# Kernel tuning notes

Hardware: AMD Instinct MI355X
Metric: run time of the kernel (lower is better)

## Reference

```python
import jax, jax.numpy as jnp
import numpy as np

EPS = 1e-5  # pyg LayerNorm default eps


def _graph_ln(x):
    # pyg.nn.norm.LayerNorm(affine=False), default mode='graph', batch=None:
    # normalizes over ALL elements of the tensor (x - x.mean()) / x.std(unbiased=False)
    m = x.mean()
    v = jnp.mean((x - m) ** 2)
    return (x - m) * jax.lax.rsqrt(v + EPS)


def _cheb_conv(x, row, col, w, W, b):
    # ChebConv, normalization='sym', lambda_max=2 => scaled Laplacian
    # L_hat = L - I = -D^{-1/2} A D^{-1/2} (self-loops removed, weighted)
    # x: [B,N,C_in], row/col: [E], w: [E], W: [K,C_in,C_out], b: [C_out]
    N = x.shape[1]
    w = jnp.where(row == col, 0.0, w)  # remove_self_loops
    deg = jnp.zeros((N,), x.dtype).at[row].add(w)
    dinv = jnp.where(deg > 0, jax.lax.rsqrt(jnp.maximum(deg, 1e-12)), 0.0)
    norm = -(dinv[row] * w * dinv[col])  # [E]

    def prop(t):  # out[i] += norm_e * t[j] for edge (j=row -> i=col)
        msg = norm[None, :, None] * t[:, row, :]  # [B,E,C]
        return jnp.zeros_like(t).at[:, col, :].add(msg)

    Tx0 = x
    out = jnp.einsum('bnc,cd->bnd', Tx0, W[0])
    Tx1 = prop(x)
    out = out + jnp.einsum('bnc,cd->bnd', Tx1, W[1])
    for k in range(2, W.shape[0]):
        Tx2 = 2.0 * prop(Tx1) - Tx0
        out = out + jnp.einsum('bnc,cd->bnd', Tx2, W[k])
        Tx0, Tx1 = Tx1, Tx2
    return out + b


def setup_inputs() -> dict:
    key = jax.random.key(0)
    ks = jax.random.split(key, 8)
    B, N, C, E, L, K = 8, 2048, 256, 32768, 3, 3
    node_feature = jax.random.normal(ks[0], (B, N, C), dtype=jnp.float32)
    edge_index = jax.random.randint(ks[1], (L, 2, E), 0, N)
    edge_weight = jax.random.uniform(ks[2], (L, E), dtype=jnp.float32)
    s = 1.0 / np.sqrt(C)
    cheb_w = jax.random.normal(ks[3], (L, K, C, C), dtype=jnp.float32) * s
    cheb_b = jnp.zeros((L, C), dtype=jnp.float32)
    mlp_w = jax.random.normal(ks[4], (L, C, C), dtype=jnp.float32) * s
    mlp_b = jax.random.normal(ks[5], (L, C), dtype=jnp.float32) * 0.01
    return {"node_feature": node_feature, "edge_weight": edge_weight,
            "cheb_w": cheb_w, "cheb_b": cheb_b, "mlp_w": mlp_w,
            "mlp_b": mlp_b, "edge_index": edge_index}


def reference(node_feature, edge_weight, cheb_w, cheb_b, mlp_w, mlp_b, edge_index):
    h = node_feature  # [B,N,C]
    L = cheb_w.shape[0]
    for l in range(L):
        h_res = h
        hn = _graph_ln(h)
        hc = _cheb_conv(hn, edge_index[l, 0], edge_index[l, 1],
                        edge_weight[l], cheb_w[l], cheb_b[l])
        h = hc + h_res
        h_res = h
        hn = _graph_ln(h)
        hm = jax.nn.gelu(jnp.einsum('bnc,cd->bnd', hn, mlp_w[l]) + mlp_b[l],
                         approximate=False)  # dropout is identity at inference
        h = hm + h_res
    return h.mean(axis=1)  # [B,C]
```

## Files before the change

### kernel.cpp

```cpp
#include <hip/hip_runtime.h>

#define BATCH   8
#define NNODE   2048
#define CH      256
#define NEDGE   32768
#define NLAYER  3
#define MROWS   (NNODE*BATCH)
#define KCAT    (3*CH)
#define NTOT    (MROWS*CH)

typedef _Float16 half8 __attribute__((ext_vector_type(8)));
typedef _Float16 half4 __attribute__((ext_vector_type(4)));
typedef float    f32x4 __attribute__((ext_vector_type(4)));

#define OFF_ACAT   ((size_t)0)
#define OFF_HF     ((size_t)25165824)
#define OFF_WT     ((size_t)33554432)
#define OFF_MT     ((size_t)34734080)
#define OFF_PARTA  ((size_t)35127296)
#define OFF_PARTB  ((size_t)35135488)
#define OFF_CS     ((size_t)35143680)
#define OFF_CSM    ((size_t)35152896)
#define OFF_DEG    ((size_t)35155968)
#define OFF_CNT    ((size_t)35180544)
#define OFF_ELIST  ((size_t)35205120)
#define OFF_NORM   ((size_t)36777984)
#define OFF_R1     ((size_t)37171200)
#define OFF_R2     ((size_t)37195776)
#define OFF_MP     ((size_t)37220352)

__device__ __forceinline__ void async_lds16(const void* g, void* l) {
  __builtin_amdgcn_global_load_lds((const __attribute__((address_space(1))) void*)g,
                                   (__attribute__((address_space(3))) void*)l, 16, 0, 0);
}

__global__ __launch_bounds__(256) void k_init(const float* __restrict__ x,
                                              _Float16* __restrict__ Acat,
                                              float2* __restrict__ part,
                                              const float* __restrict__ cheb_w,
                                              const float* __restrict__ mlp_w,
                                              _Float16* __restrict__ Wt,
                                              _Float16* __restrict__ Mt,
                                              float* __restrict__ deg,
                                              unsigned int* __restrict__ count,
                                              float* __restrict__ r1) {
  __shared__ float rs[512];
  __shared__ _Float16 lt[64][72];
  const int blk = blockIdx.x, t = threadIdx.x;
  if (blk < 1024) {
    int tid = blk*256 + t;
    float s = 0.f, s2 = 0.f;
    for (int i = tid; i < NTOT/4; i += 1024*256) {
      int c4 = i & 63, b = (i >> 6) & 7, n = i >> 9;
      float4 v = ((const float4*)x)[((b*NNODE + n) << 6) + c4];
      half4 o; o[0]=(_Float16)v.x; o[1]=(_Float16)v.y; o[2]=(_Float16)v.z; o[3]=(_Float16)v.w;
      *(half4*)&Acat[(size_t)(i >> 6)*KCAT + c4*4] = o;
      s  += v.x + v.y + v.z + v.w;
      s2 += v.x*v.x + v.y*v.y + v.z*v.z + v.w*v.w;
    }
    rs[t] = s; rs[256+t] = s2; __syncthreads();
    for (int o = 128; o > 0; o >>= 1) {
      if (t < o) { rs[t] += rs[t+o]; rs[256+t] += rs[256+t+o]; }
      __syncthreads();
    }
    if (t == 0) part[blk] = make_float2(rs[0], rs[256]);
  } else if (blk < 1048) {
    int i = (blk - 1024)*256 + t;
    if (i < NLAYER*NNODE) { deg[i] = 0.f; count[i] = 0u; r1[i] = 0.f; }
  } else {
    const int tile = blk - 1048;
    const int rr = t >> 4, c4 = t & 15;
    if (tile < 144) {
      const int l = tile / 48, rem = tile % 48;
      const int kk = rem / 16, q = rem % 16, ci = q >> 2, ni = q & 3;
      const float4* W  = (const float4*)cheb_w + ((size_t)((l*3 + kk)*CH + ci*64))*64 + ni*16;
      const float4* W2 = (const float4*)cheb_w + ((size_t)((l*3 + 2 )*CH + ci*64))*64 + ni*16;
      #pragma unroll
      for (int p = 0; p < 4; ++p) {
        const int r = p*16 + rr;
        float4 v = W[(size_t)r*64 + c4];
        if (kk == 0) {
          float4 v2 = W2[(size_t)r*64 + c4];
          v.x -= v2.x; v.y -= v2.y; v.z -= v2.z; v.w -= v2.w;
        } else if (kk == 2) {
          v.x *= 2.f; v.y *= 2.f; v.z *= 2.f; v.w *= 2.f;
        }
        lt[c4*4+0][r] = (_Float16)v.x; lt[c4*4+1][r] = (_Float16)v.y;
        lt[c4*4+2][r] = (_Float16)v.z; lt[c4*4+3][r] = (_Float16)v.w;
      }
      __syncthreads();
      const int nr = t >> 2, ch2 = t & 3;
      #pragma unroll
      for (int pp = 0; pp < 2; ++pp) {
        const int ch = ch2 + pp*4;
        half8 v = *(const half8*)&lt[nr][ch*8];
        *(half8*)&Wt[((size_t)(l*CH + ni*64 + nr))*KCAT + kk*256 + ci*64 + ch*8] = v;
      }
    } else {
      const int m = tile - 144;
      const int l = m / 16, q = m % 16, ci = q >> 2, ni = q & 3;
      const float4* W = (const float4*)mlp_w + ((size_t)(l*CH + ci*64))*64 + ni*16;
      #pragma unroll
      for (int p = 0; p < 4; ++p) {
        const int r = p*16 + rr;
        float4 v = W[(size_t)r*64 + c4];
        lt[c4*4+0][r] = (_Float16)v.x; lt[c4*4+1][r] = (_Float16)v.y;
        lt[c4*4+2][r] = (_Float16)v.z; lt[c4*4+3][r] = (_Float16)v.w;
      }
      __syncthreads();
      const int nr = t >> 2, ch2 = t & 3;
      #pragma unroll
      for (int pp = 0; pp < 2; ++pp) {
        const int ch = ch2 + pp*4;
        half8 v = *(const half8*)&lt[nr][ch*8];
        *(half8*)&Mt[((size_t)(l*CH + ni*64 + nr))*CH + ci*64 + ch*8] = v;
      }
    }
  }
}

__global__ __launch_bounds__(256) void k_edge_scatter(const int* __restrict__ ei,
                                                      const float* __restrict__ ew,
                                                      float* deg, unsigned int* count,
                                                      unsigned int* elist) {
  int i = blockIdx.x*256 + threadIdx.x;
  if (i >= NLAYER*NEDGE) return;
  int l = i / NEDGE, e = i % NEDGE;
  const int* rows = ei + l*2*NEDGE;
  const int* cols = rows + NEDGE;
  int r = rows[e], c = cols[e];
  float w = (r == c) ? 0.f : ew[i];
  atomicAdd(&deg[l*NNODE + r], w);
  unsigned int slot = atomicAdd(&count[l*NNODE + c], 1u);
  if (slot < 64u) elist[(size_t)(l*NNODE + c)*64 + slot] = (unsigned int)e;
}

__global__ __launch_bounds__(256) void k_edge_norm(const int* __restrict__ ei,
                                                   const float* __restrict__ ew,
                                                   const float* __restrict__ deg,
                                                   float* __restrict__ norm,
                                                   float* __restrict__ r1) {
  int i = blockIdx.x*256 + threadIdx.x;
  if (i >= NLAYER*NEDGE) return;
  int l = i / NEDGE, e = i % NEDGE;
  const int* rows = ei + l*2*NEDGE;
  const int* cols = rows + NEDGE;
  int r = rows[e], c = cols[e];
  float w = (r == c) ? 0.f : ew[i];
  float dr = deg[l*NNODE + r], dc = deg[l*NNODE + c];
  float ir = dr > 0.f ? rsqrtf(fmaxf(dr, 1e-12f)) : 0.f;
  float ic = dc > 0.f ? rsqrtf(fmaxf(dc, 1e-12f)) : 0.f;
  float nm = -(ir * w * ic);
  norm[i] = nm;
  atomicAdd(&r1[l*NNODE + c], nm);
}

__global__ __launch_bounds__(256) void k_aux(const int* __restrict__ ei,
                                             const float* __restrict__ norm,
                                             const unsigned int* __restrict__ count,
                                             const unsigned int* __restrict__ elist,
                                             const float* __restrict__ r1,
                                             float* __restrict__ r2,
                                             const _Float16* __restrict__ Wt,
                                             const _Float16* __restrict__ Mt,
                                             float* __restrict__ cs,
                                             float* __restrict__ csM) {
  const int blk = blockIdx.x;
  if (blk < 24) {
    int i = blk*256 + threadIdx.x;
    int l = i / NNODE;
    const int* rows = ei + l*2*NEDGE;
    unsigned int c = count[i]; if (c > 64u) c = 64u;
    const unsigned int* el = elist + (size_t)i*64;
    float s = 0.f;
    for (unsigned int j = 0; j < c; ++j) {
      unsigned int e = el[j];
      s += norm[l*NEDGE + e] * r1[l*NNODE + rows[e]];
    }
    r2[i] = s;
  } else if (blk < 33) {
    int idx = blk - 24;
    int l = idx / 3, kk = idx % 3, n = threadIdx.x;
    const half8* row = (const half8*)&Wt[((size_t)(l*CH + n))*KCAT + kk*256];
    float s = 0.f;
    #pragma unroll 4
    for (int j = 0; j < 32; ++j) {
      half8 v = row[j];
      s += (float)v[0]+(float)v[1]+(float)v[2]+(float)v[3]
         + (float)v[4]+(float)v[5]+(float)v[6]+(float)v[7];
    }
    cs[(l*3 + kk)*CH + n] = s;
  } else {
    int l = blk - 33, n = threadIdx.x;
    const half8* row = (const half8*)&Mt[((size_t)(l*CH + n))*CH];
    float s = 0.f;
    #pragma unroll 4
    for (int j = 0; j < 32; ++j) {
      half8 v = row[j];
      s += (float)v[0]+(float)v[1]+(float)v[2]+(float)v[3]
         + (float)v[4]+(float)v[5]+(float)v[6]+(float)v[7];
    }
    csM[l*CH + n] = s;
  }
}

template<int SRC_OFF, int DST_OFF>
__global__ __launch_bounds__(256) void k_prop(_Float16* __restrict__ Acat,
                                              const int* __restrict__ rows,
                                              const float* __restrict__ nrm,
                                              const unsigned int* __restrict__ count,
                                              const unsigned int* __restrict__ el) {
  const int g = blockIdx.x*4 + (threadIdx.x >> 6);
  const int lane = threadIdx.x & 63;
  const int dst = g >> 1, bb = (g & 1) << 2;
  unsigned int c = count[dst]; if (c > 64u) c = 64u;
  int srcv = 0; float nmv = 0.f;
  if (lane < (int)c) {
    unsigned int e = el[(size_t)dst*64 + lane];
    srcv = rows[e]; nmv = nrm[e];
  }
  float acc[4][4] = {{0.f,0.f,0.f,0.f},{0.f,0.f,0.f,0.f},{0.f,0.f,0.f,0.f},{0.f,0.f,0.f,0.f}};
  const _Float16* base = Acat + SRC_OFF + lane*4;
  for (unsigned int i = 0; i < c; ++i) {
    int   src = __builtin_amdgcn_readlane(srcv, i);
    int   nbi = __builtin_amdgcn_readlane(__builtin_bit_cast(int, nmv), i);
    float nm  = __builtin_bit_cast(float, nbi);
    const _Float16* p = base + (size_t)(src*8 + bb)*KCAT;
    #pragma unroll
    for (int j = 0; j < 4; ++j) {
      half4 v = *(const half4*)(p + (size_t)j*KCAT);
      acc[j][0] += nm*(float)v[0]; acc[j][1] += nm*(float)v[1];
      acc[j][2] += nm*(float)v[2]; acc[j][3] += nm*(float)v[3];
    }
  }
  #pragma unroll
  for (int j = 0; j < 4; ++j) {
    half4 o; o[0]=(_Float16)acc[j][0]; o[1]=(_Float16)acc[j][1];
    o[2]=(_Float16)acc[j][2]; o[3]=(_Float16)acc[j][3];
    *(half4*)&Acat[(size_t)(dst*8 + bb + j)*KCAT + DST_OFF + lane*4] = o;
  }
}

template<int KSTEPS, int DO_GELU>
__global__ __launch_bounds__(256) void k_gemm(const _Float16* __restrict__ A, int lda,
                                              const _Float16* __restrict__ Bt, int ldb,
                                              const float* __restrict__ bias,
                                              const float* __restrict__ cs,
                                              const float* __restrict__ r1,
                                              const float* __restrict__ r2,
                                              const float2* __restrict__ part_in,
                                              float2* __restrict__ part_out,
                                              const _Float16* __restrict__ R, int ldr,
                                              _Float16* __restrict__ O, int ldo) {
  __shared__ _Float16 Als[64*64];
  __shared__ _Float16 Bls[64*64];
  __shared__ float red[512];
  __shared__ float mv[2];
  const int bm = blockIdx.x, bn = blockIdx.y;
  const int t = threadIdx.x;
  const int w = t >> 6, lane = t & 63;
  const int quad = lane >> 4, l16 = lane & 15;
  const int wm = w & 1, wn = w >> 1;

  {
    float s = 0.f, s2 = 0.f;
    for (int i = t; i < 1024; i += 256) { float2 p = part_in[i]; s += p.x; s2 += p.y; }
    red[t] = s; red[256+t] = s2; __syncthreads();
    for (int o = 128; o > 0; o >>= 1) {
      if (t < o) { red[t] += red[t+o]; red[256+t] += red[256+t+o]; }
      __syncthreads();
    }
    if (t == 0) {
      float mean = red[0] * (1.f/(float)NTOT);
      float var  = red[256] * (1.f/(float)NTOT) - mean*mean;
      mv[0] = mean; mv[1] = rsqrtf(var + 1e-5f);
    }
    __syncthreads();
  }
  const float mean = mv[0], istd = mv[1];

  f32x4 acc00 = {0.f,0.f,0.f,0.f};
  f32x4 acc01 = acc00, acc10 = acc00, acc11 = acc00;

  const int c0 = w*64 + lane, c1 = 256 + w*64 + lane;
  const int r0 = c0 >> 3, s0 = (c0 & 7) ^ (r0 & 7);
  const int r1i = c1 >> 3, s1 = (c1 & 7) ^ (r1i & 7);
  const _Float16* ga0 = A  + (size_t)(bm*64 + r0)*lda + s0*8;
  const _Float16* ga1 = A  + (size_t)(bm*64 + r1i)*lda + s1*8;
  const _Float16* gb0 = Bt + (size_t)(bn*64 + r0)*ldb + s0*8;
  const _Float16* gb1 = Bt + (size_t)(bn*64 + r1i)*ldb + s1*8;
  _Float16* lA0 = &Als[w*512];
  _Float16* lA1 = &Als[2048 + w*512];
  _Float16* lB0 = &Bls[w*512];
  _Float16* lB1 = &Bls[2048 + w*512];

  const int ra0 = wm*32 + l16, ra1 = ra0 + 16;
  const int rb0 = wn*32 + l16, rb1 = rb0 + 16;

  for (int ks = 0; ks < KSTEPS; ++ks) {
    async_lds16(ga0, lA0); async_lds16(ga1, lA1);
    async_lds16(gb0, lB0); async_lds16(gb1, lB1);
    ga0 += 64; ga1 += 64; gb0 += 64; gb1 += 64;
    __syncthreads();
    #pragma unroll
    for (int kh = 0; kh < 2; ++kh) {
      const int q = kh*4 + quad;
      half8 a0 = *(const half8*)&Als[ra0*64 + (q ^ (ra0 & 7))*8];
      half8 a1 = *(const half8*)&Als[ra1*64 + (q ^ (ra1 & 7))*8];
      half8 b0 = *(const half8*)&Bls[rb0*64 + (q ^ (rb0 & 7))*8];
      half8 b1 = *(const half8*)&Bls[rb1*64 + (q ^ (rb1 & 7))*8];
      acc00 = __builtin_amdgcn_mfma_f32_16x16x32_f16(a0, b0, acc00, 0, 0, 0);
      acc01 = __builtin_amdgcn_mfma_f32_16x16x32_f16(a0, b1, acc01, 0, 0, 0);
      acc10 = __builtin_amdgcn_mfma_f32_16x16x32_f16(a1, b0, acc10, 0, 0, 0);
      acc11 = __builtin_amdgcn_mfma_f32_16x16x32_f16(a1, b1, acc11, 0, 0, 0);
    }
    __syncthreads();
  }

  float s = 0.f, s2 = 0.f;
  const int gm0 = bm*64 + wm*32, gn0 = bn*64 + wn*32;
  const float mi = -mean * istd;
  #pragma unroll
  for (int i = 0; i < 2; ++i) {
    #pragma unroll
    for (int j = 0; j < 2; ++j) {
      f32x4 a = (i == 0) ? (j == 0 ? acc00 : acc01) : (j == 0 ? acc10 : acc11);
      const int col = gn0 + j*16 + l16;
      const float bv = bias[col];
      const float c0v = cs[col];
      float c1v = 0.f, c2v = 0.f;
      if (!DO_GELU) { c1v = cs[256 + col]; c2v = cs[512 + col]; }
      #pragma unroll
      for (int r = 0; r < 4; ++r) {
        const int row = gm0 + i*16 + quad*4 + r;
        float v;
        if (DO_GELU) {
          v = istd*a[r] + mi*c0v + bv;
          v = 0.5f*v*(1.f + erff(v*0.70710678118654752f));
        } else {
          const int node = row >> 3;
          v = istd*a[r] + mi*(c0v + r1[node]*c1v + r2[node]*c2v) + bv;
        }
        float hv = (float)R[(size_t)row*ldr + col] + v;
        O[(size_t)row*ldo + col] = (_Float16)hv;
        s += hv; s2 += hv*hv;
      }
    }
  }
  red[t] = s; red[256+t] = s2; __syncthreads();
  for (int o = 128; o > 0; o >>= 1) {
    if (t < o) { red[t] += red[t+o]; red[256+t] += red[256+t+o]; }
    __syncthreads();
  }
  if (t == 0) part_out[blockIdx.y*gridDim.x + blockIdx.x] = make_float2(red[0], red[256]);
}

__global__ __launch_bounds__(256) void k_mean_part(const _Float16* __restrict__ Acat,
                                                   float* __restrict__ mp) {
  int blk = blockIdx.x;
  int b = blk & 7, chunk = blk >> 3;
  int c = threadIdx.x;
  float s = 0.f;
  for (int k = 0; k < 32; ++k) {
    int n = chunk*32 + k;
    s += (float)Acat[(size_t)(n*8 + b)*KCAT + c];
  }
  mp[((b*64 + chunk) << 8) + c] = s;
}

__global__ __launch_bounds__(256) void k_mean_final(const float* __restrict__ mp,
                                                    float* __restrict__ out) {
  int b = blockIdx.x, c = threadIdx.x;
  float s = 0.f;
  for (int ch = 0; ch < 64; ++ch) s += mp[((b*64 + ch) << 8) + c];
  out[(b << 8) + c] = s * (1.f/(float)NNODE);
}

extern "C" void kernel_launch(void* const* d_in, const int* in_sizes, int n_in,
                              void* d_out, int out_size, void* d_ws, size_t ws_size,
                              hipStream_t stream) {
  const float* x      = (const float*)d_in[0];
  const float* ew     = (const float*)d_in[1];
  const float* cheb_w = (const float*)d_in[2];
  const float* cheb_b = (const float*)d_in[3];
  const float* mlp_w  = (const float*)d_in[4];
  const float* mlp_b  = (const float*)d_in[5];
  const int*   ei     = (const int*)d_in[6];
  float* out = (float*)d_out;

  char* ws = (char*)d_ws;
  _Float16*     Acat  = (_Float16*)(ws + OFF_ACAT);
  _Float16*     Hf    = (_Float16*)(ws + OFF_HF);
  _Float16*     Wt    = (_Float16*)(ws + OFF_WT);
  _Float16*     Mt    = (_Float16*)(ws + OFF_MT);
  float2*       partA = (float2*)(ws + OFF_PARTA);
  float2*       partB = (float2*)(ws + OFF_PARTB);
  float*        cs    = (float*)(ws + OFF_CS);
  float*        csM   = (float*)(ws + OFF_CSM);
  float*        deg   = (float*)(ws + OFF_DEG);
  unsigned int* cnt   = (unsigned int*)(ws + OFF_CNT);
  unsigned int* elist = (unsigned int*)(ws + OFF_ELIST);
  float*        norm  = (float*)(ws + OFF_NORM);
  float*        r1    = (float*)(ws + OFF_R1);
  float*        r2    = (float*)(ws + OFF_R2);
  float*        mp    = (float*)(ws + OFF_MP);

  k_init<<<1240, 256, 0, stream>>>(x, Acat, partA, cheb_w, mlp_w, Wt, Mt, deg, cnt, r1);
  k_edge_scatter<<<(NLAYER*NEDGE)/256, 256, 0, stream>>>(ei, ew, deg, cnt, elist);
  k_edge_norm<<<(NLAYER*NEDGE)/256, 256, 0, stream>>>(ei, ew, deg, norm, r1);
  k_aux<<<36, 256, 0, stream>>>(ei, norm, cnt, elist, r1, r2, Wt, Mt, cs, csM);

  for (int l = 0; l < NLAYER; ++l) {
    const int* rows_l = ei + l*2*NEDGE;
    const unsigned int* cnt_l = cnt + l*NNODE;
    const unsigned int* el_l  = elist + (size_t)l*NNODE*64;
    const float* norm_l = norm + l*NEDGE;

    k_prop<0, 256><<<1024, 256, 0, stream>>>(Acat, rows_l, norm_l, cnt_l, el_l);
    k_prop<256, 512><<<1024, 256, 0, stream>>>(Acat, rows_l, norm_l, cnt_l, el_l);
    k_gemm<12, 0><<<dim3(256, 4), 256, 0, stream>>>(
        Acat, KCAT, Wt + (size_t)l*CH*KCAT, KCAT, cheb_b + l*CH,
        cs + l*3*CH, r1 + l*NNODE, r2 + l*NNODE, partA, partB,
        Acat, KCAT, Hf, CH);
    k_gemm<4, 1><<<dim3(256, 4), 256, 0, stream>>>(
        Hf, CH, Mt + (size_t)l*CH*CH, CH, mlp_b + l*CH,
        csM + l*CH, r1, r2, partB, partA,
        Hf, CH, Acat, KCAT);
  }

  k_mean_part<<<512, 256, 0, stream>>>(Acat, mp);
  k_mean_final<<<8, 256, 0, stream>>>(mp, out);
}
```

Measured before the change: 315.0 us.

## Fold aux precompute into first prop launch, remap prop per batch, atomic mean

Moves the r2, column-sum and output-zeroing work into extra blocks of the first layer's prop kernel, removing a separate launch. Each prop block now covers four destination nodes for one batch, with one node per wave, instead of four batches per wave, and the edge loop is unrolled by four to keep more gathers in flight. The final mean becomes one kernel that adds into the zeroed output with atomics instead of a two-pass reduction. The trade-off is four times as many prop blocks, with each edge list and its index loads read once per batch, and float atomics on the output.

After: 299.2 us. 1.05x faster.

```diff
diff --git a/kernel.cpp b/kernel.cpp
--- a/kernel.cpp
+++ b/kernel.cpp
@@ -27,7 +27,6 @@
 #define OFF_NORM   ((size_t)36777984)
 #define OFF_R1     ((size_t)37171200)
 #define OFF_R2     ((size_t)37195776)
-#define OFF_MP     ((size_t)37220352)
 
 __device__ __forceinline__ void async_lds16(const void* g, void* l) {
   __builtin_amdgcn_global_load_lds((const __attribute__((address_space(1))) void*)g,
@@ -155,89 +154,89 @@
   atomicAdd(&r1[l*NNODE + c], nm);
 }
 
-__global__ __launch_bounds__(256) void k_aux(const int* __restrict__ ei,
-                                             const float* __restrict__ norm,
-                                             const unsigned int* __restrict__ count,
-                                             const unsigned int* __restrict__ elist,
-                                             const float* __restrict__ r1,
-                                             float* __restrict__ r2,
-                                             const _Float16* __restrict__ Wt,
-                                             const _Float16* __restrict__ Mt,
-                                             float* __restrict__ cs,
-                                             float* __restrict__ csM) {
-  const int blk = blockIdx.x;
-  if (blk < 24) {
-    int i = blk*256 + threadIdx.x;
-    int l = i / NNODE;
-    const int* rows = ei + l*2*NEDGE;
-    unsigned int c = count[i]; if (c > 64u) c = 64u;
-    const unsigned int* el = elist + (size_t)i*64;
-    float s = 0.f;
-    for (unsigned int j = 0; j < c; ++j) {
-      unsigned int e = el[j];
-      s += norm[l*NEDGE + e] * r1[l*NNODE + rows[e]];
-    }
-    r2[i] = s;
-  } else if (blk < 33) {
-    int idx = blk - 24;
-    int l = idx / 3, kk = idx % 3, n = threadIdx.x;
-    const half8* row = (const half8*)&Wt[((size_t)(l*CH + n))*KCAT + kk*256];
-    float s = 0.f;
-    #pragma unroll 4
-    for (int j = 0; j < 32; ++j) {
-      half8 v = row[j];
-      s += (float)v[0]+(float)v[1]+(float)v[2]+(float)v[3]
-         + (float)v[4]+(float)v[5]+(float)v[6]+(float)v[7];
-    }
-    cs[(l*3 + kk)*CH + n] = s;
-  } else {
-    int l = blk - 33, n = threadIdx.x;
-    const half8* row = (const half8*)&Mt[((size_t)(l*CH + n))*CH];
-    float s = 0.f;
-    #pragma unroll 4
-    for (int j = 0; j < 32; ++j) {
-      half8 v = row[j];
-      s += (float)v[0]+(float)v[1]+(float)v[2]+(float)v[3]
-         + (float)v[4]+(float)v[5]+(float)v[6]+(float)v[7];
-    }
-    csM[l*CH + n] = s;
-  }
-}
-
-template<int SRC_OFF, int DST_OFF>
+template<int SRC_OFF, int DST_OFF, int AUX>
 __global__ __launch_bounds__(256) void k_prop(_Float16* __restrict__ Acat,
                                               const int* __restrict__ rows,
                                               const float* __restrict__ nrm,
                                               const unsigned int* __restrict__ count,
-                                              const unsigned int* __restrict__ el) {
-  const int g = blockIdx.x*4 + (threadIdx.x >> 6);
-  const int lane = threadIdx.x & 63;
-  const int dst = g >> 1, bb = (g & 1) << 2;
-  unsigned int c = count[dst]; if (c > 64u) c = 64u;
-  int srcv = 0; float nmv = 0.f;
-  if (lane < (int)c) {
-    unsigned int e = el[(size_t)dst*64 + lane];
-    srcv = rows[e]; nmv = nrm[e];
-  }
-  float acc[4][4] = {{0.f,0.f,0.f,0.f},{0.f,0.f,0.f,0.f},{0.f,0.f,0.f,0.f},{0.f,0.f,0.f,0.f}};
-  const _Float16* base = Acat + SRC_OFF + lane*4;
-  for (unsigned int i = 0; i < c; ++i) {
-    int   src = __builtin_amdgcn_readlane(srcv, i);
-    int   nbi = __builtin_amdgcn_readlane(__builtin_bit_cast(int, nmv), i);
-    float nm  = __builtin_bit_cast(float, nbi);
-    const _Float16* p = base + (size_t)(src*8 + bb)*KCAT;
-    #pragma unroll
-    for (int j = 0; j < 4; ++j) {
-      half4 v = *(const half4*)(p + (size_t)j*KCAT);
-      acc[j][0] += nm*(float)v[0]; acc[j][1] += nm*(float)v[1];
-      acc[j][2] += nm*(float)v[2]; acc[j][3] += nm*(float)v[3];
-    }
-  }
-  #pragma unroll
-  for (int j = 0; j < 4; ++j) {
-    half4 o; o[0]=(_Float16)acc[j][0]; o[1]=(_Float16)acc[j][1];
-    o[2]=(_Float16)acc[j][2]; o[3]=(_Float16)acc[j][3];
-    *(half4*)&Acat[(size_t)(dst*8 + bb + j)*KCAT + DST_OFF + lane*4] = o;
+                                              const unsigned int* __restrict__ el,
+                                              const int* __restrict__ ei,
+                                              const float* __restrict__ norm_all,
+                                              const unsigned int* __restrict__ cnt_all,
+                                              const unsigned int* __restrict__ el_all,
+                                              const float* __restrict__ r1,
+                                              float* __restrict__ r2,
+                                              const _Float16* __restrict__ Wt,
+                                              const _Float16* __restrict__ Mt,
+                                              float* __restrict__ cs,
+                                              float* __restrict__ csM,
+                                              float* __restrict__ out_zero) {
+  const int blk = blockIdx.x, t = threadIdx.x;
+  if (!AUX || blk < 4096) {
+    const int b = blk & 7, dgrp = blk >> 3;
+    const int w = t >> 6, lane = t & 63;
+    const int dst = dgrp*4 + w;
+    unsigned int c = count[dst]; if (c > 64u) c = 64u;
+    int srcv = 0; float nmv = 0.f;
+    if (lane < (int)c) {
+      unsigned int e = el[(size_t)dst*64 + lane];
+      srcv = rows[e]; nmv = nrm[e];
+    }
+    float a0 = 0.f, a1 = 0.f, a2 = 0.f, a3 = 0.f;
+    const _Float16* base = Acat + SRC_OFF + b*KCAT + lane*4;
+    #define PROP_STEP(i)                                                            \
+      {                                                                             \
+        int   src = __builtin_amdgcn_readlane(srcv, (i));                           \
+        int   nbi = __builtin_amdgcn_readlane(__builtin_bit_cast(int, nmv), (i));   \
+        float nm  = __builtin_bit_cast(float, nbi);                                 \
+        half4 v = *(const half4*)&base[(size_t)src*8*KCAT];                         \
+        a0 += nm*(float)v[0]; a1 += nm*(float)v[1];                                 \
+        a2 += nm*(float)v[2]; a3 += nm*(float)v[3];                                 \
+      }
+    unsigned int i = 0;
+    for (; i + 4 <= c; i += 4) { PROP_STEP(i) PROP_STEP(i+1) PROP_STEP(i+2) PROP_STEP(i+3) }
+    for (; i < c; ++i) { PROP_STEP(i) }
+    #undef PROP_STEP
+    half4 o; o[0] = (_Float16)a0; o[1] = (_Float16)a1; o[2] = (_Float16)a2; o[3] = (_Float16)a3;
+    *(half4*)&Acat[(size_t)(dst*8 + b)*KCAT + DST_OFF + lane*4] = o;
+  } else {
+    const int tile = blk - 4096;
+    if (tile < 24) {
+      int i = tile*256 + t, l = i / NNODE;
+      const int* rw = ei + l*2*NEDGE;
+      unsigned int c = cnt_all[i]; if (c > 64u) c = 64u;
+      const unsigned int* elp = el_all + (size_t)i*64;
+      float s = 0.f;
+      for (unsigned int j = 0; j < c; ++j) {
+        unsigned int e = elp[j];
+        s += norm_all[l*NEDGE + e] * r1[l*NNODE + rw[e]];
+      }
+      r2[i] = s;
+    } else if (tile < 33) {
+      int idx = tile - 24, l = idx / 3, kk = idx % 3, n = t;
+      const half8* row = (const half8*)&Wt[((size_t)(l*CH + n))*KCAT + kk*256];
+      float s = 0.f;
+      #pragma unroll 4
+      for (int j = 0; j < 32; ++j) {
+        half8 v = row[j];
+        s += (float)v[0]+(float)v[1]+(float)v[2]+(float)v[3]
+           + (float)v[4]+(float)v[5]+(float)v[6]+(float)v[7];
+      }
+      cs[(l*3 + kk)*CH + n] = s;
+    } else if (tile < 36) {
+      int l = tile - 33, n = t;
+      const half8* row = (const half8*)&Mt[((size_t)(l*CH + n))*CH];
+      float s = 0.f;
+      #pragma unroll 4
+      for (int j = 0; j < 32; ++j) {
+        half8 v = row[j];
+        s += (float)v[0]+(float)v[1]+(float)v[2]+(float)v[3]
+           + (float)v[4]+(float)v[5]+(float)v[6]+(float)v[7];
+      }
+      csM[l*CH + n] = s;
+    } else {
+      for (int i = t; i < BATCH*CH; i += 256) out_zero[i] = 0.f;
+    }
   }
 }
 
@@ -355,25 +354,16 @@
   if (t == 0) part_out[blockIdx.y*gridDim.x + blockIdx.x] = make_float2(red[0], red[256]);
 }
 
-__global__ __launch_bounds__(256) void k_mean_part(const _Float16* __restrict__ Acat,
-                                                   float* __restrict__ mp) {
-  int blk = blockIdx.x;
-  int b = blk & 7, chunk = blk >> 3;
+__global__ __launch_bounds__(256) void k_mean(const _Float16* __restrict__ Acat,
+                                              float* __restrict__ out) {
+  int b = blockIdx.x & 7, chunk = blockIdx.x >> 3;
   int c = threadIdx.x;
   float s = 0.f;
-  for (int k = 0; k < 32; ++k) {
-    int n = chunk*32 + k;
+  for (int k = 0; k < 256; ++k) {
+    int n = chunk*256 + k;
     s += (float)Acat[(size_t)(n*8 + b)*KCAT + c];
   }
-  mp[((b*64 + chunk) << 8) + c] = s;
-}
-
-__global__ __launch_bounds__(256) void k_mean_final(const float* __restrict__ mp,
-                                                    float* __restrict__ out) {
-  int b = blockIdx.x, c = threadIdx.x;
-  float s = 0.f;
-  for (int ch = 0; ch < 64; ++ch) s += mp[((b*64 + ch) << 8) + c];
-  out[(b << 8) + c] = s * (1.f/(float)NNODE);
+  atomicAdd(&out[(b << 8) + c], s * (1.f/(float)NNODE));
 }
 
 extern "C" void kernel_launch(void* const* d_in, const int* in_sizes, int n_in,
@@ -403,12 +393,10 @@
   float*        norm  = (float*)(ws + OFF_NORM);
   float*        r1    = (float*)(ws + OFF_R1);
   float*        r2    = (float*)(ws + OFF_R2);
-  float*        mp    = (float*)(ws + OFF_MP);
 
   k_init<<<1240, 256, 0, stream>>>(x, Acat, partA, cheb_w, mlp_w, Wt, Mt, deg, cnt, r1);
   k_edge_scatter<<<(NLAYER*NEDGE)/256, 256, 0, stream>>>(ei, ew, deg, cnt, elist);
   k_edge_norm<<<(NLAYER*NEDGE)/256, 256, 0, stream>>>(ei, ew, deg, norm, r1);
-  k_aux<<<36, 256, 0, stream>>>(ei, norm, cnt, elist, r1, r2, Wt, Mt, cs, csM);
 
   for (int l = 0; l < NLAYER; ++l) {
     const int* rows_l = ei + l*2*NEDGE;
@@ -416,8 +404,18 @@
     const unsigned int* el_l  = elist + (size_t)l*NNODE*64;
     const float* norm_l = norm + l*NEDGE;
 
-    k_prop<0, 256><<<1024, 256, 0, stream>>>(Acat, rows_l, norm_l, cnt_l, el_l);
-    k_prop<256, 512><<<1024, 256, 0, stream>>>(Acat, rows_l, norm_l, cnt_l, el_l);
+    if (l == 0) {
+      k_prop<0, 256, 1><<<4133, 256, 0, stream>>>(
+          Acat, rows_l, norm_l, cnt_l, el_l,
+          ei, norm, cnt, elist, r1, r2, Wt, Mt, cs, csM, out);
+    } else {
+      k_prop<0, 256, 0><<<4096, 256, 0, stream>>>(
+          Acat, rows_l, norm_l, cnt_l, el_l,
+          ei, norm, cnt, elist, r1, r2, Wt, Mt, cs, csM, out);
+    }
+    k_prop<256, 512, 0><<<4096, 256, 0, stream>>>(
+        Acat, rows_l, norm_l, cnt_l, el_l,
+        ei, norm, cnt, elist, r1, r2, Wt, Mt, cs, csM, out);
     k_gemm<12, 0><<<dim3(256, 4), 256, 0, stream>>>(
         Acat, KCAT, Wt + (size_t)l*CH*KCAT, KCAT, cheb_b + l*CH,
         cs + l*3*CH, r1 + l*NNODE, r2 + l*NNODE, partA, partB,
@@ -428,6 +426,5 @@
         Hf, CH, Acat, KCAT);
   }
 
-  k_mean_part<<<512, 256, 0, stream>>>(Acat, mp);
-  k_mean_final<<<8, 256, 0, stream>>>(mp, out);
-}
+  k_mean<<<64, 256, 0, stream>>>(Acat, out);
+}
```
